# Optimization experiments

Measured on AMD Instinct MI355X. Metric: run time of the kernel, lower is better.

Reference implementation:

```python
import jax, jax.numpy as jnp
import numpy as np

H_PARAM = 3.0   # filtering strength h
TWS = 5         # template window size
SWS = 11        # search window size


def _shift_stack(x, window_size):
    # [N,C,H,W] -> [N,C,H,W,window_size**2] of circularly shifted copies.
    # Shift order matches the torch module: outer loop x_shift, inner y_shift,
    # roll shifts=(y_shift, x_shift) on dims (H, W).
    r = window_size // 2
    return jnp.stack(
        [jnp.roll(x, (ys, xs), axis=(2, 3))
         for xs in range(-r, r + 1) for ys in range(-r, r + 1)],
        axis=-1,
    )


def _box_filter(x, window_size):
    # Circular box-sum over H,W dims. The torch double roll loop is separable,
    # so do it as two 1-D roll sums (10 rolls instead of 25 for tws=5).
    r = window_size // 2
    s = x
    acc = x
    for k in range(1, r + 1):
        acc = acc + jnp.roll(s, k, axis=3) + jnp.roll(s, -k, axis=3)
    s2 = acc
    for k in range(1, r + 1):
        acc = acc + jnp.roll(s2, k, axis=2) + jnp.roll(s2, -k, axis=2)
    return acc


def setup_inputs() -> dict:
    key = jax.random.key(0)
    x = jax.random.uniform(key, (2, 3, 512, 512), dtype=jnp.float32)
    return {"x": x}


def reference(x):
    # luminance (RGB input: C == 3)
    xc = jnp.clip(x, 0.0, 1.0)
    y = 0.299 * xc[:, :1] + 0.587 * xc[:, 1:2] + 0.114 * xc[:, 2:3]  # [N,1,H,W]

    x_stack = _shift_stack(x, SWS)  # [N,3,H,W,sws^2]
    y_stack = _shift_stack(y, SWS)  # [N,1,H,W,sws^2]

    d2 = _box_filter((y[..., None] - y_stack) ** 2, TWS)  # [N,1,H,W,sws^2]
    distances = jnp.sqrt(d2)
    weights = jnp.exp(-distances / H_PARAM)                # [N,1,H,W,sws^2]

    denoised = (weights * x_stack).sum(axis=-1) / weights.sum(axis=-1)
    return jnp.clip(denoised, 0.0, 1.0)
```

## Files before the change

kernel.cpp:

```cpp
#include <hip/hip_runtime.h>
#include <math.h>


#define H_IMG 512
#define W_IMG 512
#define MASK  511
#define HWSZ  (H_IMG * W_IMG)
#define TILE  32
#define HALO  7
#define XD    46
#define YSTR  48
#define HSTR  44
#define VSTR  44

typedef _Float16 h2 __attribute__((ext_vector_type(2)));
typedef float f32x2 __attribute__((ext_vector_type(2)));

__device__ __forceinline__ float fdot2(h2 a, h2 b, float c) {
#if __has_builtin(__builtin_amdgcn_fdot2)
    return __builtin_amdgcn_fdot2(a, b, c, false);
#else
    return c + (float)a.x * (float)b.x + (float)a.y * (float)b.y;
#endif
}

__device__ __forceinline__ float fast_exp2(float x) {
#if __has_builtin(__builtin_amdgcn_exp2f)
    return __builtin_amdgcn_exp2f(x);
#else
    return __expf(x * 0.6931471805599453f);
#endif
}

#define K2C   0.23126321070979063f
#define N2K2 -0.46252642141958126f

__global__ __launch_bounds__(256, 2)
void nlm_kernel(const float* __restrict__ x, float* __restrict__ out) {
    __shared__ float4   ldsX[XD * XD];
    __shared__ float    ldsYf[XD * YSTR];
    __shared__ unsigned ldsY2[XD * YSTR];
    __shared__ float    ldsH[XD * HSTR];
    __shared__ float    ldsV[42 * VSTR];

    const int n  = blockIdx.z;
    const int ti = blockIdx.y * TILE;
    const int tj = blockIdx.x * TILE;
    const int tx = threadIdx.x;
    const int ty = threadIdx.y;
    const int tid = ty * 32 + tx;

    const float* xb = x + (size_t)n * 3 * HWSZ;

    for (int e = tid; e < XD * XD; e += 256) {
        int r = e / XD, c = e - r * XD;
        int gi = (ti + r - HALO) & MASK;
        int gj = (tj + c - HALO) & MASK;
        size_t o = (size_t)gi * W_IMG + gj;
        ldsX[e] = make_float4(xb[o], xb[o + HWSZ], xb[o + 2 * HWSZ], 0.f);
    }
    __syncthreads();

    for (int e = tid; e < XD * 47; e += 256) {
        int r = e / 47, c = e - r * 47;
        int cs = (c == 46) ? 45 : c;
        float4 v = ldsX[r * XD + cs];
        float rr = fminf(fmaxf(v.x, 0.f), 1.f);
        float gg = fminf(fmaxf(v.y, 0.f), 1.f);
        float bb = fminf(fmaxf(v.z, 0.f), 1.f);
        ldsYf[r * YSTR + c] = 0.299f * rr + 0.587f * gg + 0.114f * bb;
    }
    __syncthreads();

    for (int e = tid; e < XD * XD; e += 256) {
        int r = e / XD, c = e - r * XD;
        h2 p;
        p.x = (_Float16)ldsYf[r * YSTR + c];
        p.y = (_Float16)ldsYf[r * YSTR + c + 1];
        ldsY2[r * YSTR + c] = __builtin_bit_cast(unsigned, p);
    }
    __syncthreads();

    for (int e = tid; e < XD * 42; e += 256) {
        int r = e / 42, c = e - r * 42;
        h2 a  = __builtin_bit_cast(h2, ldsY2[r * YSTR + c]);
        h2 b  = __builtin_bit_cast(h2, ldsY2[r * YSTR + c + 2]);
        h2 cc = __builtin_bit_cast(h2, ldsY2[r * YSTR + c + 4]);
        float x0 = (float)a.x, x1 = (float)a.y;
        float x2 = (float)b.x, x3 = (float)b.y;
        float x4 = (float)cc.x;
        ldsH[r * HSTR + c] = x0*x0 + x1*x1 + x2*x2 + x3*x3 + x4*x4;
    }
    __syncthreads();

    for (int e = tid; e < 42 * 42; e += 256) {
        int r = e / 42, c = e - r * 42;
        const float* hp = &ldsH[r * HSTR + c];
        float s = ((hp[0] + hp[HSTR]) + (hp[2*HSTR] + hp[3*HSTR])) + hp[4*HSTR];
        ldsV[r * VSTR + c] = K2C * s;
    }
    __syncthreads();

    const int jl = tx + HALO;
    const int il = ty * 4 + HALO;

    h2 cyP[8][3];
    float Vc[4];
    #pragma unroll
    for (int t = 0; t < 8; ++t) {
        int base = (il - 2 + t) * YSTR + (jl - 2);
        cyP[t][0] = __builtin_bit_cast(h2, ldsY2[base]);
        cyP[t][1] = __builtin_bit_cast(h2, ldsY2[base + 2]);
        h2 z = __builtin_bit_cast(h2, ldsY2[base + 4]);
        z.y = (_Float16)0.f;
        cyP[t][2] = z;
    }
    #pragma unroll
    for (int o = 0; o < 4; ++o)
        Vc[o] = ldsV[(il - 2 + o) * VSTR + (jl - 2)];

    f32x2 acc01[4];
    float num2[4], den[4];
    #pragma unroll
    for (int o = 0; o < 4; ++o) {
        acc01[o] = (f32x2){0.f, 0.f};
        num2[o] = 0.f; den[o] = 0.f;
    }

    #pragma unroll 1
    for (int xs = -5; xs <= 5; ++xs) {
        const int jc  = jl - xs - 2;
        const int xjc = jl - xs;

        h2     swP[8][3];
        float  Wr[4];
        float4 xw[4];

        #pragma unroll
        for (int t = 0; t < 8; ++t) {
            int base = (il - 7 + t) * YSTR + jc;
            swP[t][0] = __builtin_bit_cast(h2, ldsY2[base]);
            swP[t][1] = __builtin_bit_cast(h2, ldsY2[base + 2]);
            swP[t][2] = __builtin_bit_cast(h2, ldsY2[base + 4]);
        }
        #pragma unroll
        for (int t = 0; t < 4; ++t) {
            Wr[t] = ldsV[(il - 7 + t) * VSTR + jc];
            xw[t] = ldsX[(il - 5 + t) * XD + xjc];
        }

        float  pd2[4];
        float4 pxv;

        #pragma unroll
        for (int k = 0; k <= 10; ++k) {
            h2 nsw0, nsw1, nsw2; float nWv; float4 nxw;
            if (k < 10) {
                const int nr = il + k + 1;
                int base = nr * YSTR + jc;
                nsw0 = __builtin_bit_cast(h2, ldsY2[base]);
                nsw1 = __builtin_bit_cast(h2, ldsY2[base + 2]);
                nsw2 = __builtin_bit_cast(h2, ldsY2[base + 4]);
                nWv  = ldsV[(il + k - 3) * VSTR + jc];
                nxw  = ldsX[(il + k - 1) * XD + xjc];
            }

            float s[8];
            #pragma unroll
            for (int t = 0; t < 8; ++t) {
                const int m = (t + k) & 7;
                s[t] = fdot2(cyP[t][0], swP[m][0],
                       fdot2(cyP[t][1], swP[m][1],
                       fdot2(cyP[t][2], swP[m][2], 0.f)));
            }

            float S0 = ((s[0] + s[1]) + (s[2] + s[3])) + s[4];
            float S1 = S0 - s[0] + s[5];
            float S2 = S1 - s[1] + s[6];
            float S3 = S2 - s[2] + s[7];

            float d2a[4];
            d2a[0] = fmaf(N2K2, S0, Vc[0] + Wr[k & 3]);
            d2a[1] = fmaf(N2K2, S1, Vc[1] + Wr[(k + 1) & 3]);
            d2a[2] = fmaf(N2K2, S2, Vc[2] + Wr[(k + 2) & 3]);
            d2a[3] = fmaf(N2K2, S3, Vc[3] + Wr[(k + 3) & 3]);

            if (k > 0) {
                #pragma unroll
                for (int o = 0; o < 4; ++o) {
                    float4 xv = (o == 0) ? pxv : xw[(k - 1 + o) & 3];
                    float sd = __builtin_amdgcn_sqrtf(__builtin_fabsf(pd2[o]));
                    float w  = fast_exp2(-sd);
                    f32x2 bw = {w, w};
                    f32x2 xv01 = {xv.x, xv.y};
                    acc01[o] = __builtin_elementwise_fma(bw, xv01, acc01[o]);
                    num2[o] = fmaf(w, xv.z, num2[o]);
                    den[o] += w;
                }
            }

            #pragma unroll
            for (int o = 0; o < 4; ++o) pd2[o] = d2a[o];
            if (k < 10) {
                pxv = xw[k & 3];
                swP[k & 7][0] = nsw0;
                swP[k & 7][1] = nsw1;
                swP[k & 7][2] = nsw2;
                Wr[k & 3] = nWv;
                xw[k & 3] = nxw;
            }
        }

        #pragma unroll
        for (int o = 0; o < 4; ++o) {
            float4 xv = xw[(10 + o) & 3];
            float sd = __builtin_amdgcn_sqrtf(__builtin_fabsf(pd2[o]));
            float w  = fast_exp2(-sd);
            f32x2 bw = {w, w};
            f32x2 xv01 = {xv.x, xv.y};
            acc01[o] = __builtin_elementwise_fma(bw, xv01, acc01[o]);
            num2[o] = fmaf(w, xv.z, num2[o]);
            den[o] += w;
        }
    }

    float* ob = out + (size_t)n * 3 * HWSZ;
    #pragma unroll
    for (int o = 0; o < 4; ++o) {
        int gi = ti + ty * 4 + o;
        int gj = tj + tx;
        size_t off = (size_t)gi * W_IMG + gj;
        float inv = __builtin_amdgcn_rcpf(den[o]);
        float v0 = fminf(fmaxf(acc01[o].x * inv, 0.f), 1.f);
        float v1 = fminf(fmaxf(acc01[o].y * inv, 0.f), 1.f);
        float v2 = fminf(fmaxf(num2[o]   * inv, 0.f), 1.f);
        ob[off]            = v0;
        ob[off + HWSZ]     = v1;
        ob[off + 2 * HWSZ] = v2;
    }
}

extern "C" void kernel_launch(void* const* d_in, const int* in_sizes, int n_in,
                              void* d_out, int out_size, void* d_ws, size_t ws_size,
                              hipStream_t stream) {
    const float* x = (const float*)d_in[0];
    float* out = (float*)d_out;
    dim3 grid(W_IMG / TILE, H_IMG / TILE, 2);
    dim3 block(32, 8);
    nlm_kernel<<<grid, block, 0, stream>>>(x, out);
}
```

Baseline: 98.46 us.

## Split search-window columns across two thread slices with LDS reduction

Result: slower. 179.0 us (+81.8%).

```diff
diff --git a/kernel.cpp b/kernel.cpp
--- a/kernel.cpp
+++ b/kernel.cpp
@@ -35,7 +35,7 @@
 #define K2C   0.23126321070979063f
 #define N2K2 -0.46252642141958126f
 
-__global__ __launch_bounds__(256, 2)
+__global__ __launch_bounds__(512, 4)
 void nlm_kernel(const float* __restrict__ x, float* __restrict__ out) {
     __shared__ float4   ldsX[XD * XD];
     __shared__ float    ldsYf[XD * YSTR];
@@ -48,11 +48,12 @@
     const int tj = blockIdx.x * TILE;
     const int tx = threadIdx.x;
     const int ty = threadIdx.y;
-    const int tid = ty * 32 + tx;
+    const int tz = threadIdx.z;
+    const int tid = tz * 256 + ty * 32 + tx;
 
     const float* xb = x + (size_t)n * 3 * HWSZ;
 
-    for (int e = tid; e < XD * XD; e += 256) {
+    for (int e = tid; e < XD * XD; e += 512) {
         int r = e / XD, c = e - r * XD;
         int gi = (ti + r - HALO) & MASK;
         int gj = (tj + c - HALO) & MASK;
@@ -61,7 +62,7 @@
     }
     __syncthreads();
 
-    for (int e = tid; e < XD * 47; e += 256) {
+    for (int e = tid; e < XD * 47; e += 512) {
         int r = e / 47, c = e - r * 47;
         int cs = (c == 46) ? 45 : c;
         float4 v = ldsX[r * XD + cs];
@@ -72,7 +73,7 @@
     }
     __syncthreads();
 
-    for (int e = tid; e < XD * XD; e += 256) {
+    for (int e = tid; e < XD * XD; e += 512) {
         int r = e / XD, c = e - r * XD;
         h2 p;
         p.x = (_Float16)ldsYf[r * YSTR + c];
@@ -81,7 +82,7 @@
     }
     __syncthreads();
 
-    for (int e = tid; e < XD * 42; e += 256) {
+    for (int e = tid; e < XD * 42; e += 512) {
         int r = e / 42, c = e - r * 42;
         h2 a  = __builtin_bit_cast(h2, ldsY2[r * YSTR + c]);
         h2 b  = __builtin_bit_cast(h2, ldsY2[r * YSTR + c + 2]);
@@ -93,7 +94,7 @@
     }
     __syncthreads();
 
-    for (int e = tid; e < 42 * 42; e += 256) {
+    for (int e = tid; e < 42 * 42; e += 512) {
         int r = e / 42, c = e - r * 42;
         const float* hp = &ldsH[r * HSTR + c];
         float s = ((hp[0] + hp[HSTR]) + (hp[2*HSTR] + hp[3*HSTR])) + hp[4*HSTR];
@@ -127,8 +128,11 @@
         num2[o] = 0.f; den[o] = 0.f;
     }
 
+    const int xs_lo = tz ? 1 : -5;
+    const int xs_hi = tz ? 5 : 0;
+
     #pragma unroll 1
-    for (int xs = -5; xs <= 5; ++xs) {
+    for (int xs = xs_lo; xs <= xs_hi; ++xs) {
         const int jc  = jl - xs - 2;
         const int xjc = jl - xs;
 
@@ -224,19 +228,36 @@
         }
     }
 
-    float* ob = out + (size_t)n * 3 * HWSZ;
-    #pragma unroll
-    for (int o = 0; o < 4; ++o) {
-        int gi = ti + ty * 4 + o;
-        int gj = tj + tx;
-        size_t off = (size_t)gi * W_IMG + gj;
-        float inv = __builtin_amdgcn_rcpf(den[o]);
-        float v0 = fminf(fmaxf(acc01[o].x * inv, 0.f), 1.f);
-        float v1 = fminf(fmaxf(acc01[o].y * inv, 0.f), 1.f);
-        float v2 = fminf(fmaxf(num2[o]   * inv, 0.f), 1.f);
-        ob[off]            = v0;
-        ob[off + HWSZ]     = v1;
-        ob[off + 2 * HWSZ] = v2;
+    __syncthreads();
+    float4* red = (float4*)ldsX;
+    const int t = ty * 32 + tx;
+    if (tz == 1) {
+        #pragma unroll
+        for (int o = 0; o < 4; ++o)
+            red[o * 256 + t] = make_float4(acc01[o].x, acc01[o].y, num2[o], den[o]);
+    }
+    __syncthreads();
+
+    if (tz == 0) {
+        float* ob = out + (size_t)n * 3 * HWSZ;
+        #pragma unroll
+        for (int o = 0; o < 4; ++o) {
+            float4 p = red[o * 256 + t];
+            float n0 = acc01[o].x + p.x;
+            float n1 = acc01[o].y + p.y;
+            float n2 = num2[o] + p.z;
+            float dn = den[o] + p.w;
+            int gi = ti + ty * 4 + o;
+            int gj = tj + tx;
+            size_t off = (size_t)gi * W_IMG + gj;
+            float inv = __builtin_amdgcn_rcpf(dn);
+            float v0 = fminf(fmaxf(n0 * inv, 0.f), 1.f);
+            float v1 = fminf(fmaxf(n1 * inv, 0.f), 1.f);
+            float v2 = fminf(fmaxf(n2 * inv, 0.f), 1.f);
+            ob[off]            = v0;
+            ob[off + HWSZ]     = v1;
+            ob[off + 2 * HWSZ] = v2;
+        }
     }
 }
 
@@ -246,6 +267,6 @@
     const float* x = (const float*)d_in[0];
     float* out = (float*)d_out;
     dim3 grid(W_IMG / TILE, H_IMG / TILE, 2);
-    dim3 block(32, 8);
+    dim3 block(32, 8, 2);
     nlm_kernel<<<grid, block, 0, stream>>>(x, out);
 }
```
